# Optimization experiments

Measured on AMD Instinct MI355X. Metric: run time of the kernel, lower is better.

## Reference

```python
import jax, jax.numpy as jnp
import numpy as np

WIN_SIZE = 48
N_EVENTS = 2_000_000
D_IN, D_OUT = 64, 128
BATCH_NUM = 4096


def setup_inputs() -> dict:
    key = jax.random.key(0)
    k1, k2, k3, k4, k5 = jax.random.split(key, 5)
    return {
        "input": jax.random.normal(k1, (N_EVENTS, D_IN), dtype=jnp.float32),
        "W": jax.random.normal(k2, (D_IN, D_OUT), dtype=jnp.float32) * 0.05,
        "b": jax.random.normal(k3, (D_OUT,), dtype=jnp.float32) * 0.05,
        "batch_num": BATCH_NUM,
        "batch_i": jax.random.randint(k4, (N_EVENTS,), 0, BATCH_NUM, dtype=jnp.int32),
        "win_i": jax.random.randint(k5, (N_EVENTS,), 0, WIN_SIZE, dtype=jnp.int32),
    }


def reference(input, W, b, batch_num, batch_i, win_i):
    # embeds_model: Linear  -> [N, D_OUT]
    embeds = input @ W + b
    # flatten (batch, window) into a single segment id
    seg = batch_i * WIN_SIZE + win_i  # [N]
    num_segments = batch_num * WIN_SIZE
    sums = jax.ops.segment_sum(embeds, seg, num_segments=num_segments)  # [B*W, D]
    counts = jax.ops.segment_sum(
        jnp.ones((embeds.shape[0],), dtype=embeds.dtype), seg, num_segments=num_segments
    )[:, None]  # [B*W, 1]
    # mean where count>0, zeros elsewhere (matches masked in-place divide)
    mean = jnp.where(counts > 0, sums / jnp.maximum(counts, 1.0), 0.0)
    out = mean.reshape(batch_num, WIN_SIZE, -1)  # [B, W, D]
    return out.transpose(0, 2, 1)  # permute(0, 2, 1) -> [B, D, W]
```

## Files before the change

kernel.cpp:

```cpp
#include <hip/hip_runtime.h>


constexpr int D_IN  = 64;
constexpr int D_OUT = 128;
constexpr int WIN   = 48;
constexpr int BATCH = 4096;
constexpr int SEGS  = BATCH * WIN;
constexpr int CAP   = 48;

__global__ void k_fill(const int* __restrict__ bi, const int* __restrict__ wi,
                       int* __restrict__ cnt, int* __restrict__ lst, int n) {
    int i = blockIdx.x * blockDim.x + threadIdx.x;
    if (i >= n) return;
    int seg = bi[i] * WIN + wi[i];
    int slot = atomicAdd(&cnt[seg], 1);
    if (slot < CAP) lst[seg * CAP + slot] = i;
}

__global__ void k_gather(const float* __restrict__ inp, const int* __restrict__ cnt,
                         const int* __restrict__ lst, float* __restrict__ meang) {
    int seg = blockIdx.x * (blockDim.x >> 6) + (threadIdx.x >> 6);
    if (seg >= SEGS) return;
    int lane = threadIdx.x & 63;
    int c = cnt[seg];
    int m = c < CAP ? c : CAP;
    int ev = 0;
    if (lane < m) ev = lst[seg * CAP + lane];
    int sub = lane >> 4;
    int ch  = lane & 15;
    float ax = 0.f, ay = 0.f, az = 0.f, aw = 0.f;
    int i = 0;
    for (; i + 8 <= m; i += 8) {
        int eA = __shfl(ev, i + sub);
        int eB = __shfl(ev, i + 4 + sub);
        const float4 vA = *(const float4*)(inp + (size_t)eA * D_IN + ch * 4);
        const float4 vB = *(const float4*)(inp + (size_t)eB * D_IN + ch * 4);
        ax += vA.x + vB.x; ay += vA.y + vB.y; az += vA.z + vB.z; aw += vA.w + vB.w;
    }
    if (i + 4 <= m) {
        int e = __shfl(ev, i + sub);
        const float4 v = *(const float4*)(inp + (size_t)e * D_IN + ch * 4);
        ax += v.x; ay += v.y; az += v.z; aw += v.w;
        i += 4;
    }
    int rem = m - i;
    if (rem > 0) {
        int idx = i + (sub < rem ? sub : rem - 1);
        int e = __shfl(ev, idx);
        const float4 v = *(const float4*)(inp + (size_t)e * D_IN + ch * 4);
        if (sub < rem) { ax += v.x; ay += v.y; az += v.z; aw += v.w; }
    }
    ax += __shfl_xor(ax, 16); ax += __shfl_xor(ax, 32);
    ay += __shfl_xor(ay, 16); ay += __shfl_xor(ay, 32);
    az += __shfl_xor(az, 16); az += __shfl_xor(az, 32);
    aw += __shfl_xor(aw, 16); aw += __shfl_xor(aw, 32);
    if (sub == 0) {
        float inv = c > 0 ? 1.0f / (float)c : 0.0f;
        float4 o; o.x = ax * inv; o.y = ay * inv; o.z = az * inv; o.w = aw * inv;
        *(float4*)(meang + (size_t)seg * D_IN + ch * 4) = o;
    }
}

__global__ __launch_bounds__(192) void k_gemm(const float* __restrict__ meang,
                                              const int* __restrict__ cnt,
                                              const float* __restrict__ Wg,
                                              const float* __restrict__ bg,
                                              float* __restrict__ out) {
    __shared__ __attribute__((aligned(16))) float sMean[64 * 100];
    __shared__ __attribute__((aligned(16))) float sW[64 * 128];
    __shared__ float sBias[D_OUT];
    __shared__ int sCnt[96];
    int tid = threadIdx.x;
    int blk = blockIdx.x;
    int s0 = blk * 96;

    for (int idx = tid; idx < (64 * 128) / 4; idx += 192)
        ((float4*)sW)[idx] = ((const float4*)Wg)[idx];
    for (int t = tid; t < 96 * 16; t += 192) {
        int sl = t >> 4, c4 = t & 15;
        const float4 v = *(const float4*)(meang + (size_t)(s0 + sl) * 64 + c4 * 4);
        sMean[(4 * c4 + 0) * 100 + sl] = v.x;
        sMean[(4 * c4 + 1) * 100 + sl] = v.y;
        sMean[(4 * c4 + 2) * 100 + sl] = v.z;
        sMean[(4 * c4 + 3) * 100 + sl] = v.w;
    }
    if (tid < D_OUT) sBias[tid] = bg[tid];
    if (tid < 96) sCnt[tid] = cnt[s0 + tid];
    __syncthreads();

    int tw = tid % 12, td = tid / 12;
    int w0 = tw * 8, d0 = td * 8;
    float acc[8][8];
#pragma unroll
    for (int x = 0; x < 8; x++)
#pragma unroll
        for (int y = 0; y < 8; y++) acc[x][y] = 0.f;

    for (int k = 0; k < 64; ++k) {
        const float4 a0 = *(const float4*)&sMean[k * 100 + w0];
        const float4 a1 = *(const float4*)&sMean[k * 100 + w0 + 4];
        const float4 b0 = *(const float4*)&sW[k * 128 + d0];
        const float4 b1 = *(const float4*)&sW[k * 128 + d0 + 4];
        float av[8] = {a0.x, a0.y, a0.z, a0.w, a1.x, a1.y, a1.z, a1.w};
        float bv[8] = {b0.x, b0.y, b0.z, b0.w, b1.x, b1.y, b1.z, b1.w};
#pragma unroll
        for (int x = 0; x < 8; x++)
#pragma unroll
            for (int y = 0; y < 8; y++)
                acc[x][y] += av[x] * bv[y];
    }

#pragma unroll
    for (int x = 0; x < 8; x++) {
        int wl = w0 + x;
        int hi = wl >= WIN ? 1 : 0;
        int ww = wl - hi * WIN;
        float flag = sCnt[wl] > 0 ? 1.f : 0.f;
        size_t obase = ((size_t)(blk * 2 + hi) * D_OUT + d0) * WIN + ww;
#pragma unroll
        for (int y = 0; y < 8; y++)
            out[obase + (size_t)y * WIN] = flag * (acc[x][y] + sBias[d0 + y]);
    }
}

extern "C" void kernel_launch(void* const* d_in, const int* in_sizes, int n_in,
                              void* d_out, int out_size, void* d_ws, size_t ws_size,
                              hipStream_t stream) {
    const float* inp = (const float*)d_in[0];
    const float* Wg  = (const float*)d_in[1];
    const float* bg  = (const float*)d_in[2];
    const int* bi = (const int*)d_in[4];
    const int* wi = (const int*)d_in[5];
    float* out = (float*)d_out;
    int n = in_sizes[0] / D_IN;

    char* ws = (char*)d_ws;
    int*   cnt   = (int*)ws;
    int*   lst   = (int*)(ws + (size_t)SEGS * 4);
    float* meang = (float*)(ws + (size_t)SEGS * 4 + (size_t)SEGS * CAP * 4);

    hipMemsetAsync(cnt, 0, (size_t)SEGS * 4, stream);
    k_fill<<<(n + 255) / 256, 256, 0, stream>>>(bi, wi, cnt, lst, n);
    k_gather<<<SEGS / 4, 256, 0, stream>>>(inp, cnt, lst, meang);
    k_gemm<<<BATCH / 2, 192, 0, stream>>>(meang, cnt, Wg, bg, out);
}
```

Measured before the change: 932.8 us.

## Fuse segment gather-mean with GEMM in one per-batch kernel

Merges the gather/mean kernel and the GEMM kernel into one kernel with one block per batch. Each of 6 wavefronts averages 8 windows and writes the means straight into transposed shared memory, prefetching the next segment's event list as it goes. This removes the global round trip and the extra launch for the intermediate mean buffer. The GEMM tile shrinks to 4x4 per thread and outputs are written as float4, and the list writes in the fill kernel become nontemporal stores. The costs are more serial gather work per wavefront and a full W load into shared memory for every batch, now 4096 blocks instead of 2048.

```diff
diff --git a/kernel.cpp b/kernel.cpp
--- a/kernel.cpp
+++ b/kernel.cpp
@@ -7,6 +7,7 @@
 constexpr int BATCH = 4096;
 constexpr int SEGS  = BATCH * WIN;
 constexpr int CAP   = 48;
+constexpr int SMS   = 52;
 
 __global__ void k_fill(const int* __restrict__ bi, const int* __restrict__ wi,
                        int* __restrict__ cnt, int* __restrict__ lst, int n) {
@@ -14,112 +15,119 @@
     if (i >= n) return;
     int seg = bi[i] * WIN + wi[i];
     int slot = atomicAdd(&cnt[seg], 1);
-    if (slot < CAP) lst[seg * CAP + slot] = i;
+    if (slot < CAP) __builtin_nontemporal_store(i, &lst[(size_t)seg * CAP + slot]);
 }
 
-__global__ void k_gather(const float* __restrict__ inp, const int* __restrict__ cnt,
-                         const int* __restrict__ lst, float* __restrict__ meang) {
-    int seg = blockIdx.x * (blockDim.x >> 6) + (threadIdx.x >> 6);
-    if (seg >= SEGS) return;
-    int lane = threadIdx.x & 63;
-    int c = cnt[seg];
-    int m = c < CAP ? c : CAP;
-    int ev = 0;
-    if (lane < m) ev = lst[seg * CAP + lane];
-    int sub = lane >> 4;
-    int ch  = lane & 15;
-    float ax = 0.f, ay = 0.f, az = 0.f, aw = 0.f;
-    int i = 0;
-    for (; i + 8 <= m; i += 8) {
-        int eA = __shfl(ev, i + sub);
-        int eB = __shfl(ev, i + 4 + sub);
-        const float4 vA = *(const float4*)(inp + (size_t)eA * D_IN + ch * 4);
-        const float4 vB = *(const float4*)(inp + (size_t)eB * D_IN + ch * 4);
-        ax += vA.x + vB.x; ay += vA.y + vB.y; az += vA.z + vB.z; aw += vA.w + vB.w;
-    }
-    if (i + 4 <= m) {
-        int e = __shfl(ev, i + sub);
-        const float4 v = *(const float4*)(inp + (size_t)e * D_IN + ch * 4);
-        ax += v.x; ay += v.y; az += v.z; aw += v.w;
-        i += 4;
-    }
-    int rem = m - i;
-    if (rem > 0) {
-        int idx = i + (sub < rem ? sub : rem - 1);
-        int e = __shfl(ev, idx);
-        const float4 v = *(const float4*)(inp + (size_t)e * D_IN + ch * 4);
-        if (sub < rem) { ax += v.x; ay += v.y; az += v.z; aw += v.w; }
-    }
-    ax += __shfl_xor(ax, 16); ax += __shfl_xor(ax, 32);
-    ay += __shfl_xor(ay, 16); ay += __shfl_xor(ay, 32);
-    az += __shfl_xor(az, 16); az += __shfl_xor(az, 32);
-    aw += __shfl_xor(aw, 16); aw += __shfl_xor(aw, 32);
-    if (sub == 0) {
-        float inv = c > 0 ? 1.0f / (float)c : 0.0f;
-        float4 o; o.x = ax * inv; o.y = ay * inv; o.z = az * inv; o.w = aw * inv;
-        *(float4*)(meang + (size_t)seg * D_IN + ch * 4) = o;
-    }
-}
-
-__global__ __launch_bounds__(192) void k_gemm(const float* __restrict__ meang,
-                                              const int* __restrict__ cnt,
-                                              const float* __restrict__ Wg,
-                                              const float* __restrict__ bg,
-                                              float* __restrict__ out) {
-    __shared__ __attribute__((aligned(16))) float sMean[64 * 100];
+__global__ __launch_bounds__(384) void k_fused(const float* __restrict__ inp,
+                                               const int* __restrict__ cnt,
+                                               const int* __restrict__ lst,
+                                               const float* __restrict__ Wg,
+                                               const float* __restrict__ bg,
+                                               float* __restrict__ out) {
+    __shared__ __attribute__((aligned(16))) float sMeanT[64 * SMS];
     __shared__ __attribute__((aligned(16))) float sW[64 * 128];
     __shared__ float sBias[D_OUT];
-    __shared__ int sCnt[96];
-    int tid = threadIdx.x;
-    int blk = blockIdx.x;
-    int s0 = blk * 96;
+    __shared__ int   sCnt[WIN];
 
-    for (int idx = tid; idx < (64 * 128) / 4; idx += 192)
+    const int tid  = threadIdx.x;
+    const int b    = blockIdx.x;
+    const int wv   = tid >> 6;
+    const int lane = tid & 63;
+    const int sub  = lane >> 4;
+    const int ch   = lane & 15;
+
+    for (int idx = tid; idx < (64 * 128) / 4; idx += 384)
         ((float4*)sW)[idx] = ((const float4*)Wg)[idx];
-    for (int t = tid; t < 96 * 16; t += 192) {
-        int sl = t >> 4, c4 = t & 15;
-        const float4 v = *(const float4*)(meang + (size_t)(s0 + sl) * 64 + c4 * 4);
-        sMean[(4 * c4 + 0) * 100 + sl] = v.x;
-        sMean[(4 * c4 + 1) * 100 + sl] = v.y;
-        sMean[(4 * c4 + 2) * 100 + sl] = v.z;
-        sMean[(4 * c4 + 3) * 100 + sl] = v.w;
+    if (tid < D_OUT) sBias[tid] = bg[tid];
+
+    const int segBase = b * WIN + wv * 8;
+    int cl = 0;
+    if (lane < 8) cl = cnt[segBase + lane];
+
+    int mP = min(__shfl(cl, 0), CAP);
+    int evP = 0;
+    if (lane < mP) evP = lst[(size_t)segBase * CAP + lane];
+
+    for (int j = 0; j < 8; ++j) {
+        const int c  = __shfl(cl, j);
+        const int m  = c < CAP ? c : CAP;
+        const int ev = evP;
+        if (j < 7) {
+            int mn = min(__shfl(cl, j + 1), CAP);
+            evP = 0;
+            if (lane < mn) evP = lst[(size_t)(segBase + j + 1) * CAP + lane];
+        }
+        float ax = 0.f, ay = 0.f, az = 0.f, aw = 0.f;
+        int i = 0;
+        for (; i + 8 <= m; i += 8) {
+            int eA = __shfl(ev, i + sub);
+            int eB = __shfl(ev, i + 4 + sub);
+            const float4 vA = *(const float4*)(inp + (size_t)eA * D_IN + ch * 4);
+            const float4 vB = *(const float4*)(inp + (size_t)eB * D_IN + ch * 4);
+            ax += vA.x + vB.x; ay += vA.y + vB.y; az += vA.z + vB.z; aw += vA.w + vB.w;
+        }
+        if (i + 4 <= m) {
+            int e = __shfl(ev, i + sub);
+            const float4 v = *(const float4*)(inp + (size_t)e * D_IN + ch * 4);
+            ax += v.x; ay += v.y; az += v.z; aw += v.w;
+            i += 4;
+        }
+        int rem = m - i;
+        if (rem > 0) {
+            int idx = i + (sub < rem ? sub : rem - 1);
+            int e = __shfl(ev, idx);
+            const float4 v = *(const float4*)(inp + (size_t)e * D_IN + ch * 4);
+            if (sub < rem) { ax += v.x; ay += v.y; az += v.z; aw += v.w; }
+        }
+        ax += __shfl_xor(ax, 16); ax += __shfl_xor(ax, 32);
+        ay += __shfl_xor(ay, 16); ay += __shfl_xor(ay, 32);
+        az += __shfl_xor(az, 16); az += __shfl_xor(az, 32);
+        aw += __shfl_xor(aw, 16); aw += __shfl_xor(aw, 32);
+        if (sub == 0) {
+            const int w = wv * 8 + j;
+            const float inv = c > 0 ? 1.0f / (float)c : 0.0f;
+            sMeanT[(4 * ch + 0) * SMS + w] = ax * inv;
+            sMeanT[(4 * ch + 1) * SMS + w] = ay * inv;
+            sMeanT[(4 * ch + 2) * SMS + w] = az * inv;
+            sMeanT[(4 * ch + 3) * SMS + w] = aw * inv;
+            if (ch == 0) sCnt[w] = c;
+        }
     }
-    if (tid < D_OUT) sBias[tid] = bg[tid];
-    if (tid < 96) sCnt[tid] = cnt[s0 + tid];
     __syncthreads();
 
-    int tw = tid % 12, td = tid / 12;
-    int w0 = tw * 8, d0 = td * 8;
-    float acc[8][8];
+    const int tw = tid % 12, td = tid / 12;
+    const int w0 = tw * 4, d0 = td * 4;
+    float acc[4][4];
 #pragma unroll
-    for (int x = 0; x < 8; x++)
+    for (int x = 0; x < 4; x++)
 #pragma unroll
-        for (int y = 0; y < 8; y++) acc[x][y] = 0.f;
+        for (int y = 0; y < 4; y++) acc[x][y] = 0.f;
 
+#pragma unroll 4
     for (int k = 0; k < 64; ++k) {
-        const float4 a0 = *(const float4*)&sMean[k * 100 + w0];
-        const float4 a1 = *(const float4*)&sMean[k * 100 + w0 + 4];
-        const float4 b0 = *(const float4*)&sW[k * 128 + d0];
-        const float4 b1 = *(const float4*)&sW[k * 128 + d0 + 4];
-        float av[8] = {a0.x, a0.y, a0.z, a0.w, a1.x, a1.y, a1.z, a1.w};
-        float bv[8] = {b0.x, b0.y, b0.z, b0.w, b1.x, b1.y, b1.z, b1.w};
+        const float4 a  = *(const float4*)&sMeanT[k * SMS + w0];
+        const float4 bv = *(const float4*)&sW[k * 128 + d0];
+        const float av[4] = {a.x, a.y, a.z, a.w};
+        const float bb[4] = {bv.x, bv.y, bv.z, bv.w};
 #pragma unroll
-        for (int x = 0; x < 8; x++)
+        for (int x = 0; x < 4; x++)
 #pragma unroll
-            for (int y = 0; y < 8; y++)
-                acc[x][y] += av[x] * bv[y];
+            for (int y = 0; y < 4; y++)
+                acc[x][y] += av[x] * bb[y];
     }
 
+    float msk[4];
 #pragma unroll
-    for (int x = 0; x < 8; x++) {
-        int wl = w0 + x;
-        int hi = wl >= WIN ? 1 : 0;
-        int ww = wl - hi * WIN;
-        float flag = sCnt[wl] > 0 ? 1.f : 0.f;
-        size_t obase = ((size_t)(blk * 2 + hi) * D_OUT + d0) * WIN + ww;
+    for (int x = 0; x < 4; x++) msk[x] = sCnt[w0 + x] > 0 ? 1.f : 0.f;
 #pragma unroll
-        for (int y = 0; y < 8; y++)
-            out[obase + (size_t)y * WIN] = flag * (acc[x][y] + sBias[d0 + y]);
+    for (int y = 0; y < 4; y++) {
+        const float bia = sBias[d0 + y];
+        float4 o;
+        o.x = msk[0] * (acc[0][y] + bia);
+        o.y = msk[1] * (acc[1][y] + bia);
+        o.z = msk[2] * (acc[2][y] + bia);
+        o.w = msk[3] * (acc[3][y] + bia);
+        *(float4*)&out[((size_t)b * D_OUT + d0 + y) * WIN + w0] = o;
     }
 }
 
@@ -132,15 +140,13 @@
     const int* bi = (const int*)d_in[4];
     const int* wi = (const int*)d_in[5];
     float* out = (float*)d_out;
-    int n = in_sizes[0] / D_IN;
+    const int n = in_sizes[0] / D_IN;
 
     char* ws = (char*)d_ws;
-    int*   cnt   = (int*)ws;
-    int*   lst   = (int*)(ws + (size_t)SEGS * 4);
-    float* meang = (float*)(ws + (size_t)SEGS * 4 + (size_t)SEGS * CAP * 4);
+    int* cnt = (int*)ws;
+    int* lst = (int*)(ws + (size_t)SEGS * 4);
 
     hipMemsetAsync(cnt, 0, (size_t)SEGS * 4, stream);
     k_fill<<<(n + 255) / 256, 256, 0, stream>>>(bi, wi, cnt, lst, n);
-    k_gather<<<SEGS / 4, 256, 0, stream>>>(inp, cnt, lst, meang);
-    k_gemm<<<BATCH / 2, 192, 0, stream>>>(meang, cnt, Wg, bg, out);
+    k_fused<<<BATCH, 384, 0, stream>>>(inp, cnt, lst, Wg, bg, out);
 }
```

Result: no change. 935.8 us (+0.3%).
